# Kernel tuning notes

Hardware: AMD Instinct MI355X
Metric: run time of the kernel (lower is better)

Reference implementation:

```python
import jax, jax.numpy as jnp
import numpy as np

B, N, DIM = 2, 16384, 512
H, D = 8, 64          # heads, dim_head
M = 64                # n_global_queries
SC, DC = 64, 64       # context slices, context_dim


def _linear(x, W, b):
    return x @ W.T + b


def setup_inputs() -> dict:
    key = jax.random.key(0)
    ks = jax.random.split(key, 12)
    def w(k, shape, fan_in):
        return jax.random.normal(k, shape, jnp.float32) / np.sqrt(fan_in)
    return {
        "x": jax.random.normal(ks[0], (B, N, DIM), jnp.float32),
        "context": jax.random.normal(ks[1], (B, H, SC, DC), jnp.float32),
        "q_global": jax.random.normal(ks[2], (1, H, M, D), jnp.float32),
        "Wx": w(ks[3], (H * D, DIM), DIM), "bx": jnp.zeros((H * D,), jnp.float32),
        "Wk": w(ks[4], (D, D), D), "bk": jnp.zeros((D,), jnp.float32),
        "Wv": w(ks[5], (D, D), D), "bv": jnp.zeros((D,), jnp.float32),
        "Wcq": w(ks[6], (D, D), D), "bcq": jnp.zeros((D,), jnp.float32),
        "Wck": w(ks[7], (D, DC), DC), "bck": jnp.zeros((D,), jnp.float32),
        "Wcv": w(ks[8], (D, DC), DC), "bcv": jnp.zeros((D,), jnp.float32),
        "state_mixing": jnp.zeros((), jnp.float32),
        "Wo": w(ks[9], (DIM, H * D), H * D), "bo": jnp.zeros((DIM,), jnp.float32),
    }


def reference(x, context, q_global, Wx, bx, Wk, bk, Wv, bv,
              Wcq, bcq, Wck, bck, Wcv, bcv, state_mixing, Wo, bo):
    scale = 1.0  # module uses self.scale = 1.0 (no 1/sqrt(d))
    b, n, _ = x.shape
    # in-projection: (B,N,C) -> (B,H,N,D)
    x_mid = _linear(x, Wx, bx).reshape(b, n, H, D).transpose(0, 2, 1, 3)

    # ---- FLARE low-rank self-attention (routing via M global queries) ----
    k = _linear(x_mid, Wk, bk)  # (B,H,N,D)
    v = _linear(x_mid, Wv, bv)  # (B,H,N,D)
    # encode: global queries attend over N tokens -> latent (B,H,M,D)
    enc = jax.nn.softmax(jnp.einsum('ghmd,bhnd->bhmn', q_global, k) * scale, axis=-1)
    latent = jnp.einsum('bhmn,bhnd->bhmd', enc, v)
    # decode: tokens (keys as queries) attend over M latents -> (B,H,N,D)
    dec = jax.nn.softmax(jnp.einsum('bhnd,ghmd->bhnm', k, q_global) * scale, axis=-1)
    self_attn = jnp.einsum('bhnm,bhmd->bhnd', dec, latent)

    # ---- cross-attention to geometry-aware context ----
    q = _linear(x_mid, Wcq, bcq)          # (B,H,N,D)
    kc = _linear(context, Wck, bck)       # (B,H,Sc,D)
    vc = _linear(context, Wcv, bcv)       # (B,H,Sc,D)
    attn = jax.nn.softmax(jnp.einsum('bhnd,bhsd->bhns', q, kc) * scale, axis=-1)
    cross_attn = jnp.einsum('bhns,bhsd->bhnd', attn, vc)

    # ---- sigmoid-gated mixing ----
    w = jax.nn.sigmoid(state_mixing)
    out = w * self_attn + (1.0 - w) * cross_attn  # (B,H,N,D)

    out = out.transpose(0, 2, 1, 3).reshape(b, n, H * D)
    return _linear(out, Wo, bo)  # (B,N,C); dropout=0 (eval)
```

## Files before the change

### kernel.cpp

```cpp
#include <hip/hip_runtime.h>


typedef unsigned short u16;
typedef __attribute__((ext_vector_type(4))) float  f32x4;
typedef __attribute__((ext_vector_type(4))) u16    u16x4;
typedef __attribute__((ext_vector_type(8))) __bf16 bf16x8;

__device__ __forceinline__ float bf2f(u16 u) {
    return __uint_as_float(((unsigned)u) << 16);
}
__device__ __forceinline__ u16 f2bf(float f) {
    unsigned u = __float_as_uint(f);
    u += 0x7fffu + ((u >> 16) & 1u);
    return (u16)(u >> 16);
}
__device__ __forceinline__ void gload16(const void* g, void* l) {
    __builtin_amdgcn_global_load_lds(
        (const __attribute__((address_space(1))) unsigned int*)g,
        (__attribute__((address_space(3))) unsigned int*)l, 16, 0, 0);
}

#define MASK_NONE 0x7fffffffu

template<int BM, int BN, int WMW, int WNW>
__device__ __forceinline__ void gemm_core(
    const u16* __restrict__ A, int lda, unsigned amask, int koffA,
    const u16* __restrict__ Bm, int ldb, unsigned bmask, int koffB,
    int K, int trow, int tcol,
    u16* As, u16* Bs,
    f32x4 (&acc)[BM / WMW / 16][BN / WNW / 16])
{
    constexpr int FM = BM / WMW / 16;
    constexpr int FN = BN / WNW / 16;
    const int tid  = threadIdx.x;
    const int wid  = tid >> 6, lane = tid & 63;
    const int wm   = wid % WMW, wn = wid / WMW;
    const int wr   = wm * (BM / WMW), wc = wn * (BN / WNW);
    const int lrow = lane & 15, lk = (lane >> 4) * 8;

    for (int kt = 0; kt < K; kt += 32) {
        __syncthreads();
#pragma unroll
        for (int i = 0; i < BM / 64; i++) {
            int c = i * 256 + tid;
            int row = c >> 2, kg = c & 3;
            unsigned kk = ((unsigned)(koffA + kt + kg * 8)) & amask;
            gload16(A + (size_t)(trow + row) * lda + kk, As + (size_t)c * 8);
        }
#pragma unroll
        for (int i = 0; i < BN / 64; i++) {
            int c = i * 256 + tid;
            int col = c >> 2, kg = c & 3;
            unsigned kk = ((unsigned)(koffB + kt + kg * 8)) & bmask;
            gload16(Bm + (size_t)(tcol + col) * ldb + kk, Bs + (size_t)c * 8);
        }
        __syncthreads();

        bf16x8 af[FM], bfr[FN];
#pragma unroll
        for (int fm = 0; fm < FM; fm++)
            af[fm] = *(const bf16x8*)&As[(wr + fm * 16 + lrow) * 32 + lk];
#pragma unroll
        for (int fn = 0; fn < FN; fn++)
            bfr[fn] = *(const bf16x8*)&Bs[(wc + fn * 16 + lrow) * 32 + lk];
#pragma unroll
        for (int fm = 0; fm < FM; fm++)
#pragma unroll
            for (int fn = 0; fn < FN; fn++)
                acc[fm][fn] = __builtin_amdgcn_mfma_f32_16x16x32_bf16(
                    af[fm], bfr[fn], acc[fm][fn], 0, 0, 0);
    }
}


__global__ void prep_x(const float* __restrict__ x, u16* __restrict__ xs)
{
    int t = blockIdx.x * 256 + threadIdx.x;
    int n = t >> 7, e4 = (t & 127) << 2;
    f32x4 v = *(const f32x4*)(x + (size_t)n * 512 + e4);
    u16x4 hi;
#pragma unroll
    for (int j = 0; j < 4; j++) hi[j] = f2bf(v[j]);
    *(u16x4*)(xs + (size_t)n * 512 + e4) = hi;
}

__global__ void prep_w(const float* Wk, const float* Wcq, const float* Wv,
                       const float* Wx, float* CKF, float* CQF, u16* wV)
{
    int idx = blockIdx.x * 256 + threadIdx.x;
    int which = idx >> 18;
    int rem = idx & 262143;
    int c = rem >> 9, e = rem & 511;
    int h = c >> 6, d = c & 63;
    const float* W = which == 0 ? Wk : (which == 1 ? Wcq : Wv);
    float s = 0.f;
#pragma unroll 8
    for (int j = 0; j < 64; j++)
        s += W[d * 64 + j] * Wx[(h * 64 + j) * 512 + e];
    if (which == 0)      CKF[(size_t)c * 512 + e] = s;
    else if (which == 1) CQF[(size_t)c * 512 + e] = s;
    else                 wV [(size_t)c * 512 + e] = f2bf(s);
}

__global__ void prep_bias(const float* Wk, const float* Wcq, const float* Wv,
                          const float* bk, const float* bcq, const float* bv,
                          const float* bx, float* biasKQ, float* biasV)
{
    int t = blockIdx.x * 256 + threadIdx.x;
    if (t < 1024) {
        const float* W  = (t < 512) ? Wk : Wcq;
        const float* bb = (t < 512) ? bk : bcq;
        int c = t & 511; int h = c >> 6, d = c & 63;
        float s = bb[d];
        for (int j = 0; j < 64; j++) s += W[d * 64 + j] * bx[h * 64 + j];
        biasKQ[t] = s;
    } else if (t < 1536) {
        int c = t - 1024; int h = c >> 6, d = c & 63;
        float s = bv[d];
        for (int j = 0; j < 64; j++) s += Wv[d * 64 + j] * bx[h * 64 + j];
        biasV[c] = s;
    }
}

__global__ void prep_ctx(const float* ctx, const float* Wck, const float* bck,
                         const float* Wcv, const float* bcv, const float* smix,
                         float* kcf, u16* vcT)
{
    int t = blockIdx.x * 256 + threadIdx.x;
    int bh = t >> 12, r = t & 4095;
    int s_ = r >> 6, d = r & 63;
    const float* crow = ctx + ((size_t)bh * 64 + s_) * 64;
    float kc = bck[d], vc = bcv[d];
#pragma unroll 8
    for (int e = 0; e < 64; e++) {
        float ce = crow[e];
        kc += ce * Wck[d * 64 + e];
        vc += ce * Wcv[d * 64 + e];
    }
    kcf[(size_t)bh * 4096 + s_ * 64 + d] = kc;
    float w = 1.f / (1.f + __expf(-smix[0]));
    int pos = (s_ & 15) * 4 + (s_ >> 4);
    vcT[(size_t)bh * 4096 + d * 64 + pos] = f2bf((1.f - w) * vc);
}

__global__ void prep_b2(const float* CKF, const float* CQF, const float* qg,
                        const float* kcf, const float* biasKQ, u16* BigB, float* CC)
{
    int idx = blockIdx.x * 256 + threadIdx.x;
    if (idx < 262144) {
        int hm = idx >> 9, e = idx & 511;
        int h = hm >> 6;
        float s = 0.f;
#pragma unroll 8
        for (int d = 0; d < 64; d++)
            s += CKF[(size_t)(h * 64 + d) * 512 + e] * qg[(size_t)hm * 64 + d];
        u16 hi = f2bf(s), lo = f2bf(s - bf2f(hi));
#pragma unroll
        for (int b = 0; b < 2; b++) {
            size_t base = (size_t)b * 1048576 + (size_t)hm * 1024;
            BigB[base + e]       = lo;
            BigB[base + 512 + e] = hi;
        }
    } else if (idx < 786432) {
        int i2 = idx - 262144;
        int r = i2 >> 9, e = i2 & 511;
        int b = r >> 9, hs = r & 511;
        int h = hs >> 6, s_ = hs & 63;
        float s = 0.f;
#pragma unroll 8
        for (int d = 0; d < 64; d++)
            s += CQF[(size_t)(h * 64 + d) * 512 + e]
               * kcf[(size_t)(b * 8 + h) * 4096 + s_ * 64 + d];
        u16 hi = f2bf(s), lo = f2bf(s - bf2f(hi));
        size_t base = (size_t)b * 1048576 + (size_t)(512 + hs) * 1024;
        BigB[base + e]       = lo;
        BigB[base + 512 + e] = hi;
    } else if (idx < 787968) {
        int t = idx - 786432;
        if (t < 512) {
            int h = t >> 6;
            float s = 0.f;
            for (int d = 0; d < 64; d++) s += biasKQ[h * 64 + d] * qg[(size_t)t * 64 + d];
            CC[t] = s; CC[1024 + t] = s;
        } else {
            int j = t - 512;
            int b = j >> 9, hs = j & 511;
            int h = hs >> 6, s_ = hs & 63;
            float s = 0.f;
            for (int d = 0; d < 64; d++)
                s += biasKQ[512 + h * 64 + d]
                   * kcf[(size_t)(b * 8 + h) * 4096 + s_ * 64 + d];
            CC[b * 1024 + 512 + hs] = s;
        }
    }
}

__global__ __launch_bounds__(256, 2) void k_vt(const u16* wV, const u16* xs,
                                               const float* biasV, u16* vT)
{
    __shared__ u16 As[128 * 32], Bs[128 * 32];
    f32x4 acc[4][4] = {};
    int b = blockIdx.z;
    int f = blockIdx.y * gridDim.x + blockIdx.x;
    int w = (f & 7) * 64 + (f >> 3);
    int trow = (w & 3) * 128;
    int tcol = (w >> 2) * 128;
    gemm_core<128, 128, 2, 2>(wV, 512, MASK_NONE, 0,
                              xs + (size_t)b * 8388608, 512, MASK_NONE, 0,
                              512, trow, tcol, As, Bs, acc);
    int tid = threadIdx.x, wid = tid >> 6, lane = tid & 63;
    int wr = (wid & 1) * 64, wc = (wid >> 1) * 64;
    int g = lane >> 4, li = lane & 15;
#pragma unroll
    for (int fm = 0; fm < 4; fm++)
#pragma unroll
        for (int fn = 0; fn < 4; fn++) {
            int col = tcol + wc + fn * 16 + li;
#pragma unroll
            for (int j = 0; j < 4; j++) {
                int a = trow + wr + fm * 16 + g * 4 + j;
                vT[((size_t)b * 512 + a) * 16384 + col] = f2bf(acc[fm][fn][j] + biasV[a]);
            }
        }
}

__global__ void k_L(const u16* xs, const u16* BigB, const float* CC,
                    u16* P12, float* DD)
{
    __shared__ u16 As[128 * 32], Bs[128 * 32];
    f32x4 acc[4][4] = {};
    int f = blockIdx.x;
    int w = (f & 7) * 256 + (f >> 3);
    int jt = w & 7, nb = w >> 3;
    int b = nb >> 7, ntile = nb & 127;
    int trow = ntile * 128, tcol = jt * 128;
    gemm_core<128, 128, 2, 2>(xs + (size_t)b * 8388608, 512, 511u, 0,
                              BigB + (size_t)b * 1048576, 1024, MASK_NONE, 0,
                              1024, trow, tcol, As, Bs, acc);
    int tid = threadIdx.x, wid = tid >> 6, lane = tid & 63;
    int wm = wid & 1, wn = wid >> 1;
    int wr = wm * 64, wc = wn * 64;
    int g = lane >> 4, li = lane & 15;
    float cj[4];
#pragma unroll
    for (int fn = 0; fn < 4; fn++) cj[fn] = CC[b * 1024 + tcol + wc + fn * 16 + li];

    int h = jt * 2 + wn;
#pragma unroll
    for (int fm = 0; fm < 4; fm++)
#pragma unroll
        for (int j = 0; j < 4; j++) {
            float ev[4]; float dsum = 0.f;
#pragma unroll
            for (int fn = 0; fn < 4; fn++) {
                ev[fn] = __expf(acc[fm][fn][j] + cj[fn]);
                dsum += ev[fn];
            }
            dsum += __shfl_xor(dsum, 1); dsum += __shfl_xor(dsum, 2);
            dsum += __shfl_xor(dsum, 4); dsum += __shfl_xor(dsum, 8);
            float inv = 1.f / dsum;
            int row = trow + wr + fm * 16 + g * 4 + j;
            size_t pb = ((size_t)b * 16384 + row) * 1024 + tcol + wc;
            u16x4 pk;
#pragma unroll
            for (int fn = 0; fn < 4; fn++) pk[fn] = f2bf(ev[fn] * inv);
            *(u16x4*)(P12 + pb + li * 4) = pk;
            if (jt < 4 && li == 0)
                DD[(size_t)(b * 8 + h) * 16384 + row] = dsum;
        }
}

__global__ void k_dene(const u16* P12, const float* DD, float* denp)
{
    __shared__ float denL[4][64];
    int blk = blockIdx.x;
    int bh = blk >> 4, c = blk & 15;
    int b = bh >> 3, h = bh & 7;
    int t = threadIdx.x;
    int m = t & 63, r = (t >> 6) & 3;
    float s = 0.f;
    const u16* base = P12 + (size_t)b * 16384 * 1024 + h * 64 + m;
    const float* ddb = DD + (size_t)bh * 16384;
    for (int i = 0; i < 256; i++) {
        int n = c * 1024 + i * 4 + r;
        s += bf2f(base[(size_t)n * 1024]) * ddb[n];
    }
    denL[r][m] = s;
    __syncthreads();
    if (t < 64)
        denp[(size_t)(b * 512 + h * 64 + t) * 16 + c]
            = denL[0][t] + denL[1][t] + denL[2][t] + denL[3][t];
}

__global__ __launch_bounds__(256, 2) void k_latT(const u16* vT, const u16* P12,
                                                 const float* DD, float* latp)
{
    __shared__ u16 As[64 * 32], Bs[64 * 32];
    f32x4 acc[2][2] = {};
    int ch = blockIdx.x, bh = blockIdx.z;
    int b = bh >> 3, h = bh & 7;
    int koff = ch * 1024;
    int tid = threadIdx.x, wid = tid >> 6, lane = tid & 63;
    int wr = (wid & 1) * 32, wc = (wid >> 1) * 32;
    int lrow = lane & 15, lk = (lane >> 4) * 8;
    const u16* Avt = vT + (size_t)bh * 64 * 16384;

    for (int kt = 0; kt < 1024; kt += 32) {
        __syncthreads();
        {
            int row = tid >> 2, kg = tid & 3;
            gload16(Avt + (size_t)row * 16384 + koff + kt + kg * 8, As + (size_t)tid * 8);
        }
        {
            int nl = tid & 31, m0 = (tid >> 5) * 8;
            int n = koff + kt + nl;
            const u16* src = P12 + ((size_t)b * 16384 + n) * 1024 + h * 64 + m0;
            u16x4 p0 = *(const u16x4*)src;
            u16x4 p1 = *(const u16x4*)(src + 4);
            float ddv = DD[(size_t)bh * 16384 + n];
#pragma unroll
            for (int i = 0; i < 4; i++) {
                int m = m0 + i;
                Bs[m * 32 + (nl ^ ((m & 3) << 3))] = f2bf(bf2f(p0[i]) * ddv);
            }
#pragma unroll
            for (int i = 0; i < 4; i++) {
                int m = m0 + 4 + i;
                Bs[m * 32 + (nl ^ ((m & 3) << 3))] = f2bf(bf2f(p1[i]) * ddv);
            }
        }
        __syncthreads();
        bf16x8 af[2], bfv[2];
#pragma unroll
        for (int fm = 0; fm < 2; fm++)
            af[fm] = *(const bf16x8*)&As[(wr + fm * 16 + lrow) * 32 + lk];
#pragma unroll
        for (int fn = 0; fn < 2; fn++) {
            int m = wc + fn * 16 + lrow;
            bfv[fn] = *(const bf16x8*)&Bs[m * 32 + (lk ^ ((m & 3) << 3))];
        }
#pragma unroll
        for (int fm = 0; fm < 2; fm++)
#pragma unroll
            for (int fn = 0; fn < 2; fn++)
                acc[fm][fn] = __builtin_amdgcn_mfma_f32_16x16x32_bf16(
                    af[fm], bfv[fn], acc[fm][fn], 0, 0, 0);
    }
    float* C = latp + ((size_t)ch * 16 + bh) * 4096;
    int g = lane >> 4, li = lane & 15;
#pragma unroll
    for (int fm = 0; fm < 2; fm++)
#pragma unroll
        for (int fn = 0; fn < 2; fn++)
#pragma unroll
            for (int j = 0; j < 4; j++) {
                int row = wr + fm * 16 + g * 4 + j;
                int col = wc + fn * 16 + li;
                C[row * 64 + col] = acc[fm][fn][j];
            }
}

__global__ void k_latfin(const float* latp, const float* denp, const float* smix,
                         u16* latB)
{
    int t = blockIdx.x * 256 + threadIdx.x;
    int bh = t >> 12, r = t & 4095;
    int m = r & 63;
    int b = bh >> 3, h = bh & 7;
    float w = 1.f / (1.f + __expf(-smix[0]));
    float s = 0.f;
    for (int c = 0; c < 16; c++) s += latp[((size_t)c * 16 + bh) * 4096 + r];
    float dd = 0.f;
    const float* dp = denp + (size_t)(b * 512 + h * 64 + m) * 16;
    for (int c = 0; c < 16; c++) dd += dp[c];
    latB[(size_t)bh * 4096 + r] = f2bf(w * s / dd);
}

__global__ void prep_g(const u16* latB, const u16* vcT, const float* Wo, u16* G)
{
    int idx = blockIdx.x * 256 + threadIdx.x;
    int b = idx >> 19;
    int r = idx & 524287;
    int e = r >> 10, k = r & 1023;
    int h = (k >> 6) & 7, dm = k & 63;
    const u16* src = (k < 512) ? latB : vcT;
    const float* wrow = Wo + (size_t)e * 512 + h * 64;
    const u16* sb = src + (size_t)(b * 8 + h) * 4096 + dm;
    float s = 0.f;
#pragma unroll 8
    for (int d = 0; d < 64; d++)
        s += bf2f(sb[d * 64]) * wrow[d];
    G[(size_t)b * 524288 + (size_t)e * 1024 + k] = f2bf(s);
}

__global__ __launch_bounds__(256, 2) void k_fbig(const u16* P12, const u16* G,
                                                 const float* bo, float* out)
{
    __shared__ u16 As[128 * 32], Bs[128 * 32];
    f32x4 acc[4][4] = {};
    int f = blockIdx.y * gridDim.x + blockIdx.x;
    int w = (f & 7) * 128 + (f >> 3);
    int tcol = (w & 3) * 128, trow = (w >> 2) * 128;
    int b = trow >> 14;
    gemm_core<128, 128, 2, 2>(P12, 1024, MASK_NONE, 0,
                              G + (size_t)b * 524288, 1024, MASK_NONE, 0,
                              1024, trow, tcol, As, Bs, acc);
    int tid = threadIdx.x, wid = tid >> 6, lane = tid & 63;
    int wr = (wid & 1) * 64, wc = (wid >> 1) * 64;
    int g = lane >> 4, li = lane & 15;
#pragma unroll
    for (int fm = 0; fm < 4; fm++)
#pragma unroll
        for (int fn = 0; fn < 4; fn++) {
            int col = tcol + wc + fn * 16 + li;
            float bias = bo[col];
#pragma unroll
            for (int j = 0; j < 4; j++) {
                int row = trow + wr + fm * 16 + g * 4 + j;
                out[(size_t)row * 512 + col] = acc[fm][fn][j] + bias;
            }
        }
}

static const size_t XS_OFF   = 0;
static const size_t P12_OFF  = 33554432;
static const size_t VT_OFF   = 100663296;
static const size_t CKF_OFF  = 134217728;
static const size_t CQF_OFF  = 135266304;
static const size_t WV_OFF   = 136314880;
static const size_t BIGB_OFF = 136839168;
static const size_t KCF_OFF  = 141033472;
static const size_t VCT_OFF  = 141295616;
static const size_t BKQ_OFF  = 141426688;
static const size_t BV_OFF   = 141430784;
static const size_t CC_OFF   = 141432832;
static const size_t DENP_OFF = 141441024;
static const size_t DD_OFF   = 141510656;
static const size_t LATP_OFF = 142559232;
static const size_t LATB_OFF = 146753536;
static const size_t G_OFF    = 146884608;

extern "C" void kernel_launch(void* const* d_in, const int* in_sizes, int n_in,
                              void* d_out, int out_size, void* d_ws, size_t ws_size,
                              hipStream_t stream)
{
    const float* x    = (const float*)d_in[0];
    const float* ctx  = (const float*)d_in[1];
    const float* qg   = (const float*)d_in[2];
    const float* Wx   = (const float*)d_in[3];
    const float* bx   = (const float*)d_in[4];
    const float* Wk   = (const float*)d_in[5];
    const float* bk   = (const float*)d_in[6];
    const float* Wv   = (const float*)d_in[7];
    const float* bv   = (const float*)d_in[8];
    const float* Wcq  = (const float*)d_in[9];
    const float* bcq  = (const float*)d_in[10];
    const float* Wck  = (const float*)d_in[11];
    const float* bck  = (const float*)d_in[12];
    const float* Wcv  = (const float*)d_in[13];
    const float* bcv  = (const float*)d_in[14];
    const float* smix = (const float*)d_in[15];
    const float* Wo   = (const float*)d_in[16];
    const float* bo   = (const float*)d_in[17];

    char* ws = (char*)d_ws;
    u16*   xs    = (u16*)  (ws + XS_OFF);
    u16*   P12   = (u16*)  (ws + P12_OFF);
    u16*   vT    = (u16*)  (ws + VT_OFF);
    float* CKF   = (float*)(ws + CKF_OFF);
    float* CQF   = (float*)(ws + CQF_OFF);
    u16*   wV    = (u16*)  (ws + WV_OFF);
    u16*   BigB  = (u16*)  (ws + BIGB_OFF);
    float* kcf   = (float*)(ws + KCF_OFF);
    u16*   vcT   = (u16*)  (ws + VCT_OFF);
    float* biasKQ= (float*)(ws + BKQ_OFF);
    float* biasV = (float*)(ws + BV_OFF);
    float* CC    = (float*)(ws + CC_OFF);
    float* denp  = (float*)(ws + DENP_OFF);
    float* DD    = (float*)(ws + DD_OFF);
    float* latp  = (float*)(ws + LATP_OFF);
    u16*   latB  = (u16*)  (ws + LATB_OFF);
    u16*   G     = (u16*)  (ws + G_OFF);

    prep_w   <<< 3072, 256, 0, stream>>>(Wk, Wcq, Wv, Wx, CKF, CQF, wV);
    prep_bias<<<    6, 256, 0, stream>>>(Wk, Wcq, Wv, bk, bcq, bv, bx, biasKQ, biasV);
    prep_ctx <<<  256, 256, 0, stream>>>(ctx, Wck, bck, Wcv, bcv, smix, kcf, vcT);
    prep_x   <<<16384, 256, 0, stream>>>(x, xs);
    prep_b2  <<< 3078, 256, 0, stream>>>(CKF, CQF, qg, kcf, biasKQ, BigB, CC);

    k_vt    <<<dim3(128,   4, 2), 256, 0, stream>>>(wV, xs, biasV, vT);
    k_L     <<<2048, 256, 0, stream>>>(xs, BigB, CC, P12, DD);
    k_dene  <<< 256, 256, 0, stream>>>(P12, DD, denp);
    k_latT  <<<dim3( 16,   1, 16), 256, 0, stream>>>(vT, P12, DD, latp);
    k_latfin<<< 256, 256, 0, stream>>>(latp, denp, smix, latB);
    prep_g  <<<4096, 256, 0, stream>>>(latB, vcT, Wo, G);
    k_fbig  <<<dim3(  4, 256, 1), 256, 0, stream>>>(P12, G, bo, (float*)d_out);
}
```

Before: 281.9 us.

## Coalesce denominator reduction, split latent GEMM finer, transpose latent/context-value layouts

k_dene is restructured so each thread reads two adjacent bf16 columns across 128 rows, producing 128 partial chunks per column. This replaces the strided single-element reads with coalesced 32-bit loads, and k_latfin now sums 128 partials instead of 16. k_latT splits the N reduction into 32 chunks of 512 instead of 16 of 1024, which doubles the grid and the partial sums to reduce. latB and vcT are stored transposed so prep_g can read contiguous vectors of four and use vectorized weight loads.

```diff
diff --git a/kernel.cpp b/kernel.cpp
--- a/kernel.cpp
+++ b/kernel.cpp
@@ -140,7 +140,7 @@
     kcf[(size_t)bh * 4096 + s_ * 64 + d] = kc;
     float w = 1.f / (1.f + __expf(-smix[0]));
     int pos = (s_ & 15) * 4 + (s_ >> 4);
-    vcT[(size_t)bh * 4096 + d * 64 + pos] = f2bf((1.f - w) * vc);
+    vcT[(size_t)bh * 4096 + pos * 64 + d] = f2bf((1.f - w) * vc);
 }
 
 __global__ void prep_b2(const float* CKF, const float* CQF, const float* qg,
@@ -272,24 +272,23 @@
 
 __global__ void k_dene(const u16* P12, const float* DD, float* denp)
 {
-    __shared__ float denL[4][64];
     int blk = blockIdx.x;
-    int bh = blk >> 4, c = blk & 15;
-    int b = bh >> 3, h = bh & 7;
+    int b = blk >> 7, ch = blk & 127;
     int t = threadIdx.x;
-    int m = t & 63, r = (t >> 6) & 3;
-    float s = 0.f;
-    const u16* base = P12 + (size_t)b * 16384 * 1024 + h * 64 + m;
-    const float* ddb = DD + (size_t)bh * 16384;
-    for (int i = 0; i < 256; i++) {
-        int n = c * 1024 + i * 4 + r;
-        s += bf2f(base[(size_t)n * 1024]) * ddb[n];
-    }
-    denL[r][m] = s;
-    __syncthreads();
-    if (t < 64)
-        denp[(size_t)(b * 512 + h * 64 + t) * 16 + c]
-            = denL[0][t] + denL[1][t] + denL[2][t] + denL[3][t];
+    int h = t >> 5;
+    float s0 = 0.f, s1 = 0.f;
+    const float* ddb = DD + (size_t)(b * 8 + h) * 16384;
+    const u16* base = P12 + (size_t)b * 16384 * 1024 + 2 * t;
+    int n0 = ch * 128;
+    for (int i = 0; i < 128; i++) {
+        int n = n0 + i;
+        unsigned v = *(const unsigned*)(base + (size_t)n * 1024);
+        float dd = ddb[n];
+        s0 += bf2f((u16)(v & 0xffff)) * dd;
+        s1 += bf2f((u16)(v >> 16)) * dd;
+    }
+    denp[(size_t)(b * 512 + 2 * t) * 128 + ch]     = s0;
+    denp[(size_t)(b * 512 + 2 * t + 1) * 128 + ch] = s1;
 }
 
 __global__ __launch_bounds__(256, 2) void k_latT(const u16* vT, const u16* P12,
@@ -299,13 +298,13 @@
     f32x4 acc[2][2] = {};
     int ch = blockIdx.x, bh = blockIdx.z;
     int b = bh >> 3, h = bh & 7;
-    int koff = ch * 1024;
+    int koff = ch * 512;
     int tid = threadIdx.x, wid = tid >> 6, lane = tid & 63;
     int wr = (wid & 1) * 32, wc = (wid >> 1) * 32;
     int lrow = lane & 15, lk = (lane >> 4) * 8;
     const u16* Avt = vT + (size_t)bh * 64 * 16384;
 
-    for (int kt = 0; kt < 1024; kt += 32) {
+    for (int kt = 0; kt < 512; kt += 32) {
         __syncthreads();
         {
             int row = tid >> 2, kg = tid & 3;
@@ -365,15 +364,15 @@
 {
     int t = blockIdx.x * 256 + threadIdx.x;
     int bh = t >> 12, r = t & 4095;
-    int m = r & 63;
+    int d = r >> 6, m = r & 63;
     int b = bh >> 3, h = bh & 7;
     float w = 1.f / (1.f + __expf(-smix[0]));
     float s = 0.f;
-    for (int c = 0; c < 16; c++) s += latp[((size_t)c * 16 + bh) * 4096 + r];
+    for (int c = 0; c < 32; c++) s += latp[((size_t)c * 16 + bh) * 4096 + r];
     float dd = 0.f;
-    const float* dp = denp + (size_t)(b * 512 + h * 64 + m) * 16;
-    for (int c = 0; c < 16; c++) dd += dp[c];
-    latB[(size_t)bh * 4096 + r] = f2bf(w * s / dd);
+    const float* dp = denp + (size_t)(b * 512 + h * 64 + m) * 128;
+    for (int c = 0; c < 128; c++) dd += dp[c];
+    latB[(size_t)bh * 4096 + m * 64 + d] = f2bf(w * s / dd);
 }
 
 __global__ void prep_g(const u16* latB, const u16* vcT, const float* Wo, u16* G)
@@ -385,11 +384,15 @@
     int h = (k >> 6) & 7, dm = k & 63;
     const u16* src = (k < 512) ? latB : vcT;
     const float* wrow = Wo + (size_t)e * 512 + h * 64;
-    const u16* sb = src + (size_t)(b * 8 + h) * 4096 + dm;
+    const u16* sb = src + (size_t)(b * 8 + h) * 4096 + dm * 64;
     float s = 0.f;
-#pragma unroll 8
-    for (int d = 0; d < 64; d++)
-        s += bf2f(sb[d * 64]) * wrow[d];
+#pragma unroll
+    for (int d0 = 0; d0 < 64; d0 += 4) {
+        u16x4 sv = *(const u16x4*)(sb + d0);
+        f32x4 wv = *(const f32x4*)(wrow + d0);
+        s += bf2f(sv[0]) * wv[0] + bf2f(sv[1]) * wv[1]
+           + bf2f(sv[2]) * wv[2] + bf2f(sv[3]) * wv[3];
+    }
     G[(size_t)b * 524288 + (size_t)e * 1024 + k] = f2bf(s);
 }
 
@@ -435,10 +438,10 @@
 static const size_t BV_OFF   = 141430784;
 static const size_t CC_OFF   = 141432832;
 static const size_t DENP_OFF = 141441024;
-static const size_t DD_OFF   = 141510656;
-static const size_t LATP_OFF = 142559232;
-static const size_t LATB_OFF = 146753536;
-static const size_t G_OFF    = 146884608;
+static const size_t DD_OFF   = 141965312;
+static const size_t LATP_OFF = 143013888;
+static const size_t LATB_OFF = 151402496;
+static const size_t G_OFF    = 151533568;
 
 extern "C" void kernel_launch(void* const* d_in, const int* in_sizes, int n_in,
                               void* d_out, int out_size, void* d_ws, size_t ws_size,
@@ -491,7 +494,7 @@
     k_vt    <<<dim3(128,   4, 2), 256, 0, stream>>>(wV, xs, biasV, vT);
     k_L     <<<2048, 256, 0, stream>>>(xs, BigB, CC, P12, DD);
     k_dene  <<< 256, 256, 0, stream>>>(P12, DD, denp);
-    k_latT  <<<dim3( 16,   1, 16), 256, 0, stream>>>(vT, P12, DD, latp);
+    k_latT  <<<dim3( 32,   1, 16), 256, 0, stream>>>(vT, P12, DD, latp);
     k_latfin<<< 256, 256, 0, stream>>>(latp, denp, smix, latB);
     prep_g  <<<4096, 256, 0, stream>>>(latB, vcT, Wo, G);
     k_fbig  <<<dim3(  4, 256, 1), 256, 0, stream>>>(P12, G, bo, (float*)d_out);
```

Measured after the change: 281.2 us. About the same (-0.3%).
